# Performance work log

Hardware: AMD Instinct MI355X
Metric: run time of the kernel (lower is better)

Reference implementation:

```python
import jax, jax.numpy as jnp
import numpy as np

MULT = 0.0025
EPS = 1e-6  # torch F.pairwise_distance eps added to the difference


def setup_inputs() -> dict:
    key = jax.random.key(0)
    k1, k2, k3, k4 = jax.random.split(key, 4)
    B, K, N = 256, 51, 8192
    y_hat = jax.random.uniform(k1, (B, K), dtype=jnp.float32)
    y = jax.random.uniform(k2, (B, K), dtype=jnp.float32)
    face = jax.random.normal(k3, (N, 3), dtype=jnp.float32)
    bs_tensor = jax.random.normal(k4, (K, N, 3), dtype=jnp.float32)
    return {"y_hat": y_hat, "y": y, "face": face, "bs_tensor": bs_tensor}


def _reconstruct(w, face, bs_tensor):
    # face: [N,3], bs_tensor: [K,N,3], w: [B,K] -> [B,N,3]
    # Contract over blendshape dim directly (avoids the [B,K,N,3] intermediate).
    return face[None] + jnp.einsum('bk,knd->bnd', w, bs_tensor)


def reference(y_hat, y, face, bs_tensor):
    yh_face = _reconstruct(y_hat, face, bs_tensor)  # [B,N,3]
    y_face = _reconstruct(y, face, bs_tensor)       # [B,N,3]
    # transpose(1,2) -> [B,3,N]; pairwise_distance norms over last dim (N)
    diff = jnp.swapaxes(yh_face, 1, 2) - jnp.swapaxes(y_face, 1, 2) + EPS
    dist = jnp.sqrt(jnp.sum(diff * diff, axis=-1))  # [B,3]
    return jnp.sum(dist) * MULT
```

## Files before the change

### kernel.cpp

```cpp
#include <hip/hip_runtime.h>
#include <math.h>

#define NPTS     8192
#define KDIM     51
#define KPAD     64
#define CHUNKS   64
#define CHUNK_N  128
#define MULT     0.0025f

typedef short short8  __attribute__((ext_vector_type(8)));
typedef float float4v __attribute__((ext_vector_type(4)));
typedef float float4a __attribute__((ext_vector_type(4), aligned(4)));

__device__ __forceinline__ unsigned short f32_to_bf16(float f) {
    unsigned int u = __float_as_uint(f);
    unsigned int r = u + 0x7FFFu + ((u >> 16) & 1u);
    return (unsigned short)(r >> 16);
}

__global__ __launch_bounds__(256) void pl_gram(
    const float* __restrict__ bs, float* __restrict__ partial,
    float* __restrict__ pq, unsigned int* __restrict__ ctr) {
  __shared__ unsigned short lds16[KPAD * 136];

  const int bx  = blockIdx.x;
  const int tid = threadIdx.x;

  if (bx == 192) {
    for (int i = tid; i < 768; i += 256) pq[i] = 0.0f;
    if (tid == 0) ctr[0] = 0u;
    return;
  }

  const int d   = bx / CHUNKS;
  const int n0  = (bx % CHUNKS) * CHUNK_N;

  unsigned int* lds32 = (unsigned int*)lds16;
  for (int u = tid; u < KPAD * (CHUNK_N / 2); u += 256) {
    int np = u & 63;
    int k  = u >> 6;
    float v0 = 0.0f, v1 = 0.0f;
    if (k < KDIM) {
      const float* p = bs + (size_t)k * (NPTS * 3) + (size_t)(n0 + 2 * np) * 3 + d;
      float4a f = *(const float4a*)p;
      v0 = f[0];
      v1 = f[3];
    }
    lds32[k * 68 + np] = (unsigned int)f32_to_bf16(v0) |
                         ((unsigned int)f32_to_bf16(v1) << 16);
  }
  __syncthreads();

  const int wave  = tid >> 6;
  const int lane  = tid & 63;
  const int m16   = lane & 15;
  const int quad  = lane >> 4;
  const int rbase = (wave >> 1) * 32;
  const int cbase = (wave & 1) * 32;

  float4v acc00 = {0.f, 0.f, 0.f, 0.f}, acc01 = {0.f, 0.f, 0.f, 0.f};
  float4v acc10 = {0.f, 0.f, 0.f, 0.f}, acc11 = {0.f, 0.f, 0.f, 0.f};

#pragma unroll
  for (int p0 = 0; p0 < CHUNK_N; p0 += 32) {
    const int po = p0 + quad * 8;
    short8 a0 = *(const short8*)&lds16[(rbase +      m16) * 136 + po];
    short8 a1 = *(const short8*)&lds16[(rbase + 16 + m16) * 136 + po];
    short8 b0 = *(const short8*)&lds16[(cbase +      m16) * 136 + po];
    short8 b1 = *(const short8*)&lds16[(cbase + 16 + m16) * 136 + po];
    acc00 = __builtin_amdgcn_mfma_f32_16x16x32_bf16(a0, b0, acc00, 0, 0, 0);
    acc01 = __builtin_amdgcn_mfma_f32_16x16x32_bf16(a0, b1, acc01, 0, 0, 0);
    acc10 = __builtin_amdgcn_mfma_f32_16x16x32_bf16(a1, b0, acc10, 0, 0, 0);
    acc11 = __builtin_amdgcn_mfma_f32_16x16x32_bf16(a1, b1, acc11, 0, 0, 0);
  }

  float* pout = partial + (size_t)bx * 4096;
#pragma unroll
  for (int r = 0; r < 4; ++r) {
    int row0 = rbase + quad * 4 + r;
    int col0 = cbase + m16;
    pout[row0 * 64 + col0]               = acc00[r];
    pout[row0 * 64 + (col0 + 16)]        = acc01[r];
    pout[(row0 + 16) * 64 + col0]        = acc10[r];
    pout[(row0 + 16) * 64 + (col0 + 16)] = acc11[r];
  }
}

__global__ __launch_bounds__(256) void pl_finalize(
    const float* __restrict__ partial, float* __restrict__ pq,
    unsigned int* __restrict__ ctr, const float* __restrict__ yh,
    const float* __restrict__ yv, float* __restrict__ out) {
  __shared__ __align__(16) float Gl[256];
  __shared__ __align__(16) float wl[64 * 68];
  __shared__ unsigned int lflag;
  __shared__ float redw[4];

  const int bx  = blockIdx.x;
  const int d   = bx / 52;
  const int rem = bx - d * 52;
  const int rg  = rem >> 2;
  const int b0  = (rem & 3) * 64;
  const int tid = threadIdx.x;

  {
    const float* p = partial + (size_t)(d * CHUNKS) * 4096 + rg * 256 + tid;
    float s = 0.0f;
#pragma unroll 16
    for (int c = 0; c < CHUNKS; ++c) s += p[(size_t)c * 4096];
    Gl[tid] = s;
  }

  for (int i = tid; i < 64 * KDIM; i += 256) {
    int bl = i / KDIM, k = i - bl * KDIM;
    int gi = (b0 + bl) * KDIM + k;
    wl[bl * 68 + k] = yh[gi] - yv[gi];
  }
  for (int i = tid; i < 64 * 13; i += 256) {
    int bl = i / 13, c = KDIM + (i - bl * 13);
    wl[bl * 68 + c] = 0.0f;
  }
  __syncthreads();

  {
    const int jt = tid & 15;
    const int bh = tid >> 4;
    float4v g4[4];
#pragma unroll
    for (int ri = 0; ri < 4; ++ri)
      g4[ri] = *(const float4v*)&Gl[ri * 64 + jt * 4];

#pragma unroll
    for (int bl = 0; bl < 4; ++bl) {
      const int lb = bl * 16 + bh;
      float4v wj = *(const float4v*)&wl[lb * 68 + jt * 4];
      float4v wk = *(const float4v*)&wl[lb * 68 + rg * 4];
      float pqp = 0.0f;
#pragma unroll
      for (int ri = 0; ri < 4; ++ri) {
        float t = 0.0f;
#pragma unroll
        for (int jj = 0; jj < 4; ++jj) t = fmaf(g4[ri][jj], wj[jj], t);
        pqp = fmaf(wk[ri], t, pqp);
      }
#pragma unroll
      for (int off = 1; off < 16; off <<= 1) pqp += __shfl_xor(pqp, off, 16);
      if (jt == 0) atomicAdd(&pq[d * 256 + b0 + lb], pqp);
    }
  }
  __syncthreads();

  if (tid == 0) {
    unsigned int old = __hip_atomic_fetch_add(ctr, 1u, __ATOMIC_RELEASE,
                                              __HIP_MEMORY_SCOPE_AGENT);
    lflag = (old == 155u) ? 1u : 0u;
  }
  __syncthreads();
  if (lflag == 0u) return;

  if (tid == 0)
    (void)__hip_atomic_load(ctr, __ATOMIC_ACQUIRE, __HIP_MEMORY_SCOPE_AGENT);
  __syncthreads();

  float s = 0.0f;
#pragma unroll
  for (int i = 0; i < 3; ++i) {
    float q = __hip_atomic_load(&pq[i * 256 + tid], __ATOMIC_RELAXED,
                                __HIP_MEMORY_SCOPE_AGENT);
    s += sqrtf(q);
  }
  for (int off = 32; off; off >>= 1) s += __shfl_down(s, off, 64);
  if ((tid & 63) == 0) redw[tid >> 6] = s;
  __syncthreads();
  if (tid == 0)
    out[0] = (redw[0] + redw[1] + redw[2] + redw[3]) * MULT;
}

extern "C" void kernel_launch(void* const* d_in, const int* in_sizes, int n_in,
                              void* d_out, int out_size, void* d_ws, size_t ws_size,
                              hipStream_t stream) {
  const float* y_hat = (const float*)d_in[0];
  const float* y     = (const float*)d_in[1];
  const float* bs    = (const float*)d_in[3];
  float* out = (float*)d_out;

  float* partial    = (float*)d_ws;
  float* pq         = partial + (size_t)3 * CHUNKS * 4096;
  unsigned int* ctr = (unsigned int*)(pq + 768);

  pl_gram<<<193, 256, 0, stream>>>(bs, partial, pq, ctr);
  pl_finalize<<<156, 256, 0, stream>>>(partial, pq, ctr, y_hat, y, out);
}
```

Measured before the change: 19.43 us.

## Replace Gram-matrix formulation with direct per-batch MFMA reconstruction of differences

Drops the Gram-matrix approach, which computed bs^T bs per chunk, wrote 64x64 partials to global memory and reduced them in a second kernel. The new path precomputes the weight difference split into bf16 hi and lo parts, then directly multiplies W (256x64) by each bs chunk with MFMA. It squares and accumulates the results in registers and atomically adds them into per-(d,b) sums. This removes the large partial-buffer write and readback but does about twice the MFMA work (hi and lo passes) over all 256 batches, and adds an XOR-swizzled LDS layout plus a small init kernel.

```diff
diff --git a/kernel.cpp b/kernel.cpp
--- a/kernel.cpp
+++ b/kernel.cpp
@@ -7,10 +7,11 @@
 #define CHUNKS   64
 #define CHUNK_N  128
 #define MULT     0.0025f
+#define NBLK     (3 * CHUNKS)
+#define LK       72
 
 typedef short short8  __attribute__((ext_vector_type(8)));
 typedef float float4v __attribute__((ext_vector_type(4)));
-typedef float float4a __attribute__((ext_vector_type(4), aligned(4)));
 
 __device__ __forceinline__ unsigned short f32_to_bf16(float f) {
     unsigned int u = __float_as_uint(f);
@@ -18,141 +19,130 @@
     return (unsigned short)(r >> 16);
 }
 
-__global__ __launch_bounds__(256) void pl_gram(
-    const float* __restrict__ bs, float* __restrict__ partial,
+__global__ __launch_bounds__(256) void pl_init(
+    const float* __restrict__ yh, const float* __restrict__ yv,
+    unsigned short* __restrict__ w_hi, unsigned short* __restrict__ w_lo,
     float* __restrict__ pq, unsigned int* __restrict__ ctr) {
-  __shared__ unsigned short lds16[KPAD * 136];
-
-  const int bx  = blockIdx.x;
-  const int tid = threadIdx.x;
-
-  if (bx == 192) {
-    for (int i = tid; i < 768; i += 256) pq[i] = 0.0f;
+  const int bx = blockIdx.x, tid = threadIdx.x;
+  if (bx == 8) {
+    pq[tid] = 0.0f; pq[256 + tid] = 0.0f; pq[512 + tid] = 0.0f;
     if (tid == 0) ctr[0] = 0u;
+    for (int i = tid; i < 256 * (KPAD - KDIM); i += 256) {
+      int b = i / (KPAD - KDIM), k = KDIM + i % (KPAD - KDIM);
+      w_hi[b * KPAD + k] = 0; w_lo[b * KPAD + k] = 0;
+    }
     return;
   }
-
-  const int d   = bx / CHUNKS;
-  const int n0  = (bx % CHUNKS) * CHUNK_N;
-
-  unsigned int* lds32 = (unsigned int*)lds16;
-  for (int u = tid; u < KPAD * (CHUNK_N / 2); u += 256) {
-    int np = u & 63;
-    int k  = u >> 6;
-    float v0 = 0.0f, v1 = 0.0f;
-    if (k < KDIM) {
-      const float* p = bs + (size_t)k * (NPTS * 3) + (size_t)(n0 + 2 * np) * 3 + d;
-      float4a f = *(const float4a*)p;
-      v0 = f[0];
-      v1 = f[3];
+  for (int i = tid; i < 408; i += 256) {
+    int idx4 = bx * 408 + i;
+    float4v h = *(const float4v*)&yh[idx4 * 4];
+    float4v v = *(const float4v*)&yv[idx4 * 4];
+#pragma unroll
+    for (int j = 0; j < 4; ++j) {
+      int e = idx4 * 4 + j;
+      int b = e / KDIM, k = e - b * KDIM;
+      float w = h[j] - v[j];
+      unsigned short hi = f32_to_bf16(w);
+      float lo = w - __uint_as_float((unsigned int)hi << 16);
+      w_hi[b * KPAD + k] = hi;
+      w_lo[b * KPAD + k] = f32_to_bf16(lo);
     }
-    lds32[k * 68 + np] = (unsigned int)f32_to_bf16(v0) |
-                         ((unsigned int)f32_to_bf16(v1) << 16);
-  }
-  __syncthreads();
-
-  const int wave  = tid >> 6;
-  const int lane  = tid & 63;
-  const int m16   = lane & 15;
-  const int quad  = lane >> 4;
-  const int rbase = (wave >> 1) * 32;
-  const int cbase = (wave & 1) * 32;
-
-  float4v acc00 = {0.f, 0.f, 0.f, 0.f}, acc01 = {0.f, 0.f, 0.f, 0.f};
-  float4v acc10 = {0.f, 0.f, 0.f, 0.f}, acc11 = {0.f, 0.f, 0.f, 0.f};
-
-#pragma unroll
-  for (int p0 = 0; p0 < CHUNK_N; p0 += 32) {
-    const int po = p0 + quad * 8;
-    short8 a0 = *(const short8*)&lds16[(rbase +      m16) * 136 + po];
-    short8 a1 = *(const short8*)&lds16[(rbase + 16 + m16) * 136 + po];
-    short8 b0 = *(const short8*)&lds16[(cbase +      m16) * 136 + po];
-    short8 b1 = *(const short8*)&lds16[(cbase + 16 + m16) * 136 + po];
-    acc00 = __builtin_amdgcn_mfma_f32_16x16x32_bf16(a0, b0, acc00, 0, 0, 0);
-    acc01 = __builtin_amdgcn_mfma_f32_16x16x32_bf16(a0, b1, acc01, 0, 0, 0);
-    acc10 = __builtin_amdgcn_mfma_f32_16x16x32_bf16(a1, b0, acc10, 0, 0, 0);
-    acc11 = __builtin_amdgcn_mfma_f32_16x16x32_bf16(a1, b1, acc11, 0, 0, 0);
-  }
-
-  float* pout = partial + (size_t)bx * 4096;
-#pragma unroll
-  for (int r = 0; r < 4; ++r) {
-    int row0 = rbase + quad * 4 + r;
-    int col0 = cbase + m16;
-    pout[row0 * 64 + col0]               = acc00[r];
-    pout[row0 * 64 + (col0 + 16)]        = acc01[r];
-    pout[(row0 + 16) * 64 + col0]        = acc10[r];
-    pout[(row0 + 16) * 64 + (col0 + 16)] = acc11[r];
   }
 }
 
-__global__ __launch_bounds__(256) void pl_finalize(
-    const float* __restrict__ partial, float* __restrict__ pq,
-    unsigned int* __restrict__ ctr, const float* __restrict__ yh,
-    const float* __restrict__ yv, float* __restrict__ out) {
-  __shared__ __align__(16) float Gl[256];
-  __shared__ __align__(16) float wl[64 * 68];
+__global__ __launch_bounds__(256) void pl_direct(
+    const float* __restrict__ bs,
+    const unsigned short* __restrict__ w_hi,
+    const unsigned short* __restrict__ w_lo,
+    float* __restrict__ pq, unsigned int* __restrict__ ctr,
+    float* __restrict__ out) {
+  __shared__ unsigned short bs_lds[CHUNK_N * LK];
   __shared__ unsigned int lflag;
   __shared__ float redw[4];
 
   const int bx  = blockIdx.x;
-  const int d   = bx / 52;
-  const int rem = bx - d * 52;
-  const int rg  = rem >> 2;
-  const int b0  = (rem & 3) * 64;
+  const int d   = bx / CHUNKS;
+  const int n0  = (bx % CHUNKS) * CHUNK_N;
   const int tid = threadIdx.x;
+  const int wave = tid >> 6, lane = tid & 63;
+  const int m16 = lane & 15, quad = lane >> 4;
 
-  {
-    const float* p = partial + (size_t)(d * CHUNKS) * 4096 + rg * 256 + tid;
-    float s = 0.0f;
-#pragma unroll 16
-    for (int c = 0; c < CHUNKS; ++c) s += p[(size_t)c * 4096];
-    Gl[tid] = s;
-  }
+  short8 ah[2][4], al[2][4];
+#pragma unroll
+  for (int ks = 0; ks < 2; ++ks)
+#pragma unroll
+    for (int mt = 0; mt < 4; ++mt) {
+      int off = (wave * 64 + mt * 16 + m16) * KPAD + ks * 32 + quad * 8;
+      ah[ks][mt] = *(const short8*)&w_hi[off];
+      al[ks][mt] = *(const short8*)&w_lo[off];
+    }
 
-  for (int i = tid; i < 64 * KDIM; i += 256) {
-    int bl = i / KDIM, k = i - bl * KDIM;
-    int gi = (b0 + bl) * KDIM + k;
-    wl[bl * 68 + k] = yh[gi] - yv[gi];
-  }
-  for (int i = tid; i < 64 * 13; i += 256) {
-    int bl = i / 13, c = KDIM + (i - bl * 13);
-    wl[bl * 68 + c] = 0.0f;
+  unsigned int* lds32 = (unsigned int*)bs_lds;
+#pragma unroll
+  for (int it = 0; it < 16; ++it) {
+    int u  = it * 256 + tid;
+    int n  = u & 127;
+    int kp = u >> 7;
+    int k0 = kp * 2;
+    float v0 = 0.0f, v1 = 0.0f;
+    if (k0 < KDIM) {
+      const float* p = bs + (size_t)k0 * (NPTS * 3) + (size_t)(n0 + n) * 3 + d;
+      v0 = p[0];
+      if (k0 + 1 < KDIM) v1 = p[NPTS * 3];
+    }
+    lds32[n * (LK / 2) + (kp ^ (((n >> 1) & 7) << 2))] =
+        (unsigned int)f32_to_bf16(v0) | ((unsigned int)f32_to_bf16(v1) << 16);
   }
   __syncthreads();
 
-  {
-    const int jt = tid & 15;
-    const int bh = tid >> 4;
-    float4v g4[4];
+  float qacc[4][4] = {{0.f}};
 #pragma unroll
-    for (int ri = 0; ri < 4; ++ri)
-      g4[ri] = *(const float4v*)&Gl[ri * 64 + jt * 4];
+  for (int nt = 0; nt < 8; ++nt) {
+    float4v acc[4] = {{0.f,0.f,0.f,0.f}, {0.f,0.f,0.f,0.f},
+                      {0.f,0.f,0.f,0.f}, {0.f,0.f,0.f,0.f}};
+#pragma unroll
+    for (int ks = 0; ks < 2; ++ks) {
+      const int nr = nt * 16 + m16;
+      const int kk = (ks * 32 + quad * 8) ^ (((nr >> 1) & 7) << 3);
+      short8 bf = *(const short8*)&bs_lds[nr * LK + kk];
+#pragma unroll
+      for (int mt = 0; mt < 4; ++mt)
+        acc[mt] = __builtin_amdgcn_mfma_f32_16x16x32_bf16(ah[ks][mt], bf, acc[mt], 0, 0, 0);
+#pragma unroll
+      for (int mt = 0; mt < 4; ++mt)
+        acc[mt] = __builtin_amdgcn_mfma_f32_16x16x32_bf16(al[ks][mt], bf, acc[mt], 0, 0, 0);
+    }
+#pragma unroll
+    for (int mt = 0; mt < 4; ++mt)
+#pragma unroll
+      for (int r = 0; r < 4; ++r)
+        qacc[mt][r] = fmaf(acc[mt][r], acc[mt][r], qacc[mt][r]);
+  }
 
 #pragma unroll
-    for (int bl = 0; bl < 4; ++bl) {
-      const int lb = bl * 16 + bh;
-      float4v wj = *(const float4v*)&wl[lb * 68 + jt * 4];
-      float4v wk = *(const float4v*)&wl[lb * 68 + rg * 4];
-      float pqp = 0.0f;
+  for (int mt = 0; mt < 4; ++mt)
 #pragma unroll
-      for (int ri = 0; ri < 4; ++ri) {
-        float t = 0.0f;
+    for (int r = 0; r < 4; ++r) {
+      float v = qacc[mt][r];
+      v += __shfl_xor(v, 1, 16);
+      v += __shfl_xor(v, 2, 16);
+      v += __shfl_xor(v, 4, 16);
+      v += __shfl_xor(v, 8, 16);
+      qacc[mt][r] = v;
+    }
+  if (m16 == 0) {
 #pragma unroll
-        for (int jj = 0; jj < 4; ++jj) t = fmaf(g4[ri][jj], wj[jj], t);
-        pqp = fmaf(wk[ri], t, pqp);
-      }
+    for (int mt = 0; mt < 4; ++mt)
 #pragma unroll
-      for (int off = 1; off < 16; off <<= 1) pqp += __shfl_xor(pqp, off, 16);
-      if (jt == 0) atomicAdd(&pq[d * 256 + b0 + lb], pqp);
-    }
+      for (int r = 0; r < 4; ++r)
+        atomicAdd(&pq[d * 256 + wave * 64 + mt * 16 + quad * 4 + r], qacc[mt][r]);
   }
   __syncthreads();
 
   if (tid == 0) {
     unsigned int old = __hip_atomic_fetch_add(ctr, 1u, __ATOMIC_RELEASE,
                                               __HIP_MEMORY_SCOPE_AGENT);
-    lflag = (old == 155u) ? 1u : 0u;
+    lflag = (old == (NBLK - 1)) ? 1u : 0u;
   }
   __syncthreads();
   if (lflag == 0u) return;
@@ -183,10 +173,11 @@
   const float* bs    = (const float*)d_in[3];
   float* out = (float*)d_out;
 
-  float* partial    = (float*)d_ws;
-  float* pq         = partial + (size_t)3 * CHUNKS * 4096;
-  unsigned int* ctr = (unsigned int*)(pq + 768);
+  unsigned short* w_hi = (unsigned short*)d_ws;
+  unsigned short* w_lo = w_hi + 256 * KPAD;
+  float* pq            = (float*)(w_lo + 256 * KPAD);
+  unsigned int* ctr    = (unsigned int*)(pq + 768);
 
-  pl_gram<<<193, 256, 0, stream>>>(bs, partial, pq, ctr);
-  pl_finalize<<<156, 256, 0, stream>>>(partial, pq, ctr, y_hat, y, out);
+  pl_init<<<9, 256, 0, stream>>>(y_hat, y, w_hi, w_lo, pq, ctr);
+  pl_direct<<<NBLK, 256, 0, stream>>>(bs, w_hi, w_lo, pq, ctr, y_hat  == nullptr ? out : out);
 }
```

New measurement: 27.38 us. +40.9%, slower.
